# Optimization experiments

Hardware: AMD Instinct MI355X
Metric: run time of the kernel (lower is better)

Reference implementation:

```python
import jax, jax.numpy as jnp
import numpy as np

NEG_SLOPE = 0.2
EPS = 1e-16


def _add_self_loops(edge_index, edge_weight, N):
    # PyG add_self_loops with fill_value='mean': self-loop attr = mean of
    # incoming edge attrs per node (0 if node has no incoming edges).
    src, dst = edge_index[0], edge_index[1]
    ones = jnp.ones_like(edge_weight)
    cnt = jax.ops.segment_sum(ones, dst, num_segments=N)
    wsum = jax.ops.segment_sum(edge_weight, dst, num_segments=N)
    self_w = jnp.where(cnt > 0, wsum / jnp.maximum(cnt, 1.0), 0.0)
    loop = jnp.arange(N, dtype=src.dtype)
    return (jnp.concatenate([src, loop]), jnp.concatenate([dst, loop]),
            jnp.concatenate([edge_weight, self_w]))


def _gatv2_layer(x, src, dst, ew, Wl, Wr, att, We, bias, N):
    # x: [M, N, Din]; src/dst: [E']; ew: [E']; att: [H, C]
    M = x.shape[0]
    H, C = att.shape
    xl = (x @ Wl).reshape(M, N, H, C)   # source transform (lin_l)
    xr = (x @ Wr).reshape(M, N, H, C)   # target transform (lin_r)
    xj = xl[:, src]                      # [M, E', H, C] gather source feats
    xi = xr[:, dst]                      # [M, E', H, C] gather target feats
    ee = (ew[:, None] @ We).reshape(-1, H, C)  # [E', H, C] edge embedding
    s = jax.nn.leaky_relu(xi + xj + ee[None], NEG_SLOPE)
    logits = jnp.einsum('mehc,hc->meh', s, att)  # [M, E', H]
    # segment softmax over edges grouped by destination node
    smax = jax.vmap(lambda u: jax.ops.segment_max(u, dst, num_segments=N))(logits)
    a = jnp.exp(logits - smax[:, dst])
    denom = jax.vmap(lambda u: jax.ops.segment_sum(u, dst, num_segments=N))(a)
    alpha = a / (denom[:, dst] + EPS)
    msg = alpha[..., None] * xj          # [M, E', H, C]
    out = jax.vmap(lambda u: jax.ops.segment_sum(u, dst, num_segments=N))(msg)
    return out.reshape(M, N, H * C) + bias


def setup_inputs() -> dict:
    key = jax.random.key(0)
    ks = jax.random.split(key, 14)
    B, T, N, Din = 2, 8, 5000, 64
    E, H, OUT = 80000, 2, 128
    C = OUT // H  # 64
    g = jax.nn.initializers.glorot_uniform()
    inp = {
        'x': jax.random.normal(ks[0], (B, T, N, Din), jnp.float32),
        'edge_index': jax.random.randint(ks[1], (2, E), 0, N, jnp.int32),
        'edge_weight': jax.random.uniform(ks[2], (E,), jnp.float32),
        # conv1 params
        'Wl1': g(ks[3], (Din, H * C), jnp.float32),
        'Wr1': g(ks[4], (Din, H * C), jnp.float32),
        'att1': g(ks[5], (H, C), jnp.float32),
        'We1': g(ks[6], (1, H * C), jnp.float32),
        'b1': jnp.zeros((H * C,), jnp.float32),
        # conv2 params
        'Wl2': g(ks[7], (OUT, H * C), jnp.float32),
        'Wr2': g(ks[8], (OUT, H * C), jnp.float32),
        'att2': g(ks[9], (H, C), jnp.float32),
        'We2': g(ks[10], (1, H * C), jnp.float32),
        'b2': jnp.zeros((H * C,), jnp.float32),
    }
    return inp


def reference(x, edge_index, edge_weight, Wl1, Wr1, att1, We1, b1,
              Wl2, Wr2, att2, We2, b2):
    B, T, N, Din = x.shape
    M = B * T
    # Tiling edges by B*T with node offsets is equivalent to sharing the same
    # edge list across M independent graph copies -> vectorize over M.
    src, dst, ew = _add_self_loops(edge_index, edge_weight, N)
    h = x.reshape(M, N, Din)
    h = _gatv2_layer(h, src, dst, ew, Wl1, Wr1, att1, We1, b1, N)
    h = jax.nn.elu(h)
    h = _gatv2_layer(h, src, dst, ew, Wl2, Wr2, att2, We2, b2, N)
    h = jax.nn.elu(h)
    return h.reshape(B, T, N, -1)
```

## Files before the change

kernel.cpp:

```cpp
#include <hip/hip_runtime.h>
#include <cstdint>
#include <cstddef>

static constexpr float NEG_SLOPE_C = 0.2f;
static constexpr float EPS_C = 1e-16f;
static constexpr float LOG2E_C = 1.4426950408889634f;

#if defined(__has_builtin)
#if __has_builtin(__builtin_amdgcn_exp2f)
#define EXP2F(x) __builtin_amdgcn_exp2f(x)
#else
#define EXP2F(x) exp2f(x)
#endif
#else
#define EXP2F(x) exp2f(x)
#endif

typedef __attribute__((ext_vector_type(8))) short bf16x8;
typedef __attribute__((ext_vector_type(4))) float f32x4;
typedef __attribute__((ext_vector_type(2))) float f32x2;

__device__ __forceinline__ f32x2 pk_add(f32x2 a, f32x2 b) {
    f32x2 d;
    asm("v_pk_add_f32 %0, %1, %2" : "=v"(d) : "v"(a), "v"(b));
    return d;
}
__device__ __forceinline__ f32x2 pk_mul(f32x2 a, f32x2 b) {
    f32x2 d;
    asm("v_pk_mul_f32 %0, %1, %2" : "=v"(d) : "v"(a), "v"(b));
    return d;
}
__device__ __forceinline__ f32x2 pk_fma(f32x2 a, f32x2 b, f32x2 c) {
    f32x2 d;
    asm("v_pk_fma_f32 %0, %1, %2, %3" : "=v"(d) : "v"(a), "v"(b), "v"(c));
    return d;
}
__device__ __forceinline__ f32x2 pk_abs(f32x2 a) {
    f32x2 d;
    d.x = __builtin_fabsf(a.x);
    d.y = __builtin_fabsf(a.y);
    return d;
}

__device__ __forceinline__ short bf16_rne(float x) {
    unsigned u = __float_as_uint(x);
    u = (u + 0x7FFF + ((u >> 16) & 1)) >> 16;
    return (short)u;
}
__device__ __forceinline__ float bf16f(short s) {
    return __uint_as_float(((unsigned)(unsigned short)s) << 16);
}

template<int CTRL>
__device__ __forceinline__ float dpp_add_f(float v) {
    int x = __builtin_amdgcn_update_dpp(0, __float_as_int(v), CTRL, 0xf, 0xf, true);
    return v + __int_as_float(x);
}

__device__ __forceinline__ float reduce16(float q) {
    q = dpp_add_f<0xB1>(q);
    q = dpp_add_f<0x4E>(q);
    q = dpp_add_f<0x141>(q);
    q = dpp_add_f<0x140>(q);
    return q;
}


__global__ void degree_kernel(const int* __restrict__ ei, const float* __restrict__ ew,
                              int E, int* __restrict__ cnt, float* __restrict__ wsum) {
    int e = blockIdx.x * blockDim.x + threadIdx.x;
    if (e >= E) return;
    int dst = ei[E + e];
    atomicAdd(&cnt[dst], 1);
    atomicAdd(&wsum[dst], ew[e]);
}

__global__ void scan_kernel(const int* __restrict__ cnt, const float* __restrict__ wsum,
                            int N, int E, int* __restrict__ offs, float* __restrict__ self_w) {
    __shared__ int bufA[1024];
    __shared__ int bufB[1024];
    int t = threadIdx.x;
    int chunk = (N + 1023) / 1024;
    int lo = t * chunk;
    int hi = lo + chunk; if (hi > N) hi = N; if (lo > N) lo = N;
    int s = 0;
    for (int n = lo; n < hi; ++n) s += cnt[n];
    bufA[t] = s;
    __syncthreads();
    int* srcb = bufA; int* dstb = bufB;
    for (int d = 1; d < 1024; d <<= 1) {
        int v = srcb[t];
        if (t >= d) v += srcb[t - d];
        dstb[t] = v;
        __syncthreads();
        int* tmp = srcb; srcb = dstb; dstb = tmp;
    }
    int run = (t == 0) ? 0 : srcb[t - 1];
    for (int n = lo; n < hi; ++n) { offs[n] = run; run += cnt[n]; }
    if (t == 0) offs[N] = E;
    for (int n = t; n < N; n += 1024) {
        int c = cnt[n];
        self_w[n] = (c > 0) ? (wsum[n] / (float)c) : 0.0f;
    }
}

__global__ void scatter_kernel(const int* __restrict__ ei, const float* __restrict__ ew, int E,
                               const int* __restrict__ offs, int* __restrict__ cursor,
                               int2* __restrict__ pairs) {
    int e = blockIdx.x * blockDim.x + threadIdx.x;
    if (e >= E) return;
    int dst = ei[E + e];
    int pos = offs[dst] + atomicAdd(&cursor[dst], 1);
    pairs[pos] = make_int2(ei[e] * 512, __float_as_int(ew[e]));
}


template<int K>
__global__ void wprep_kernel(const float* __restrict__ Wl, const float* __restrict__ Wr,
                             uint4* __restrict__ Wf) {
    const int gid = blockIdx.x * 256 + threadIdx.x;
    const int lane = gid & 63;
    const int t = (gid >> 6) & 15;
    const int s = gid >> 10;
    const int mr = lane & 15, q = lane >> 4;
    const int col = t * 16 + mr;
    const float* src = (col < 128) ? (Wl + col) : (Wr + col - 128);
    union { short sh[8]; uint4 u; } hv, lv;
    #pragma unroll
    for (int j = 0; j < 8; ++j) {
        const float v = src[(size_t)(s * 32 + q * 8 + j) * 128];
        const short h = bf16_rne(v);
        hv.sh[j] = h;
        lv.sh[j] = bf16_rne(v - bf16f(h));
    }
    const size_t base = (size_t)s * 2048 + (size_t)(t * 2) * 64 + lane;
    Wf[base] = hv.u;
    Wf[base + 64] = lv.u;
}


template<int K>
__global__ __launch_bounds__(256) void gemm_mfma_kernel(
    const float* __restrict__ X, const uint4* __restrict__ Wf,
    float* __restrict__ outL, float* __restrict__ outR) {
    __shared__ uint4 xbuf[8 * 64];
    const int tid = threadIdx.x;
    const int w = tid >> 6;
    const int lane = tid & 63;
    const int q = lane >> 4;
    const int mr = lane & 15;
    const int blockRow = blockIdx.x * 64;

    const int srow = lane;
    const float* sxp = X + (size_t)(blockRow + srow) * K + w * 8;
    const int sdst = ((srow >> 4) * 2) * 64 + w * 16 + (srow & 15);

    f32x4 acc[4][4];
    #pragma unroll
    for (int tt = 0; tt < 4; ++tt)
        #pragma unroll
        for (int r = 0; r < 4; ++r)
            acc[tt][r] = (f32x4){0.f, 0.f, 0.f, 0.f};

    for (int s = 0; s < K / 32; ++s) {
        const float4 a0 = *(const float4*)(sxp + s * 32);
        const float4 a1 = *(const float4*)(sxp + s * 32 + 4);
        union { short sh[8]; uint4 u; } hv, lv;
        {
            const float av[8] = {a0.x, a0.y, a0.z, a0.w, a1.x, a1.y, a1.z, a1.w};
            #pragma unroll
            for (int jj = 0; jj < 8; ++jj) {
                const short h = bf16_rne(av[jj]);
                hv.sh[jj] = h;
                lv.sh[jj] = bf16_rne(av[jj] - bf16f(h));
            }
        }
        __syncthreads();
        xbuf[sdst] = hv.u;
        xbuf[sdst + 64] = lv.u;
        __syncthreads();

        bf16x8 xh[4], xl[4];
        #pragma unroll
        for (int r = 0; r < 4; ++r) {
            xh[r] = *(const bf16x8*)&xbuf[(r * 2) * 64 + lane];
            xl[r] = *(const bf16x8*)&xbuf[(r * 2 + 1) * 64 + lane];
        }
        const uint4* wp = Wf + (size_t)s * 2048 + (size_t)(4 * w) * 128 + lane;
        #pragma unroll
        for (int tt = 0; tt < 4; ++tt) {
            const bf16x8 wh = *(const bf16x8*)&wp[tt * 128];
            const bf16x8 wl = *(const bf16x8*)&wp[tt * 128 + 64];
            #pragma unroll
            for (int r = 0; r < 4; ++r) {
                acc[tt][r] = __builtin_amdgcn_mfma_f32_16x16x32_bf16(wh, xh[r], acc[tt][r], 0, 0, 0);
                acc[tt][r] = __builtin_amdgcn_mfma_f32_16x16x32_bf16(wl, xh[r], acc[tt][r], 0, 0, 0);
                acc[tt][r] = __builtin_amdgcn_mfma_f32_16x16x32_bf16(wh, xl[r], acc[tt][r], 0, 0, 0);
            }
        }
    }

    float* const obase = (w < 2) ? outL : outR;
    const int cbase = (w & 1) * 64 + q * 4;
    #pragma unroll
    for (int tt = 0; tt < 4; ++tt) {
        #pragma unroll
        for (int r = 0; r < 4; ++r) {
            const size_t o = (size_t)(blockRow + r * 16 + mr) * 128 + cbase + tt * 16;
            *(float4*)(obase + o) =
                make_float4(acc[tt][r][0], acc[tt][r][1], acc[tt][r][2], acc[tt][r][3]);
        }
    }
}


__global__ __launch_bounds__(256) void edge_kernel(
    const float* __restrict__ xl, const float* __restrict__ xr,
    const int* __restrict__ offs, const int2* __restrict__ pairs,
    const float* __restrict__ self_w,
    const float* __restrict__ att, const float* __restrict__ We,
    const float* __restrict__ bias, float* __restrict__ out,
    int N, int M) {
    const int wave = __builtin_amdgcn_readfirstlane(threadIdx.x >> 6);
    const int b = blockIdx.x;
    const int hb = (b >= 10000) ? (b - 10000) : b;
    const int m = ((b >= 10000) ? 8 : 0) + (hb & 7);
    const int n = (hb >> 3) * 4 + wave;
    if (n >= N) return;
    const int lane = threadIdx.x & 63;
    const int j = lane & 31;
    const bool hi = lane >= 32;
    const int h4 = (lane >> 5) << 2;
    const int j16 = j << 4;

    const char* xlp = (const char*)(xl + (size_t)m * N * 128);
    const char* xrp = (const char*)(xr + (size_t)m * N * 128);

    const int beg = offs[n], end = offs[n + 1];
    const int last = end - 1;
    const bool any = end > beg;

    int2 myp;
    if (any) myp = pairs[min(beg + lane, last)];

    f32x2 a06_01, a06_23, a04_01, a04_23, we01, we23, xi01, xi23;
    {
        const float4 at4 = ((const float4*)att)[j];
        const float4 we4 = ((const float4*)We)[j];
        const float4 xi4 = *(const float4*)(xrp + (size_t)n * 512 + j16);
        const float c06 = 0.6f * LOG2E_C, c04 = 0.4f * LOG2E_C;
        a06_01 = (f32x2){at4.x * c06, at4.y * c06};
        a06_23 = (f32x2){at4.z * c06, at4.w * c06};
        a04_01 = (f32x2){at4.x * c04, at4.y * c04};
        a04_23 = (f32x2){at4.z * c04, at4.w * c04};
        we01 = (f32x2){we4.x, we4.y};
        we23 = (f32x2){we4.z, we4.w};
        xi01 = (f32x2){xi4.x, xi4.y};
        xi23 = (f32x2){xi4.z, xi4.w};
    }

    float base, lsum;
    f32x2 acc01, acc23;
    {
        const float sw = self_w[n];
        const f32x2 sw2 = (f32x2){sw, sw};
        const float4 xj4 = *(const float4*)(xlp + (size_t)n * 512 + j16);
        const f32x2 s01 = pk_fma(sw2, we01, pk_add(xi01, (f32x2){xj4.x, xj4.y}));
        const f32x2 s23 = pk_fma(sw2, we23, pk_add(xi23, (f32x2){xj4.z, xj4.w}));
        f32x2 q01 = pk_mul(a06_01, s01);
        q01 = pk_fma(a04_01, pk_abs(s01), q01);
        f32x2 q23 = pk_mul(a06_23, s23);
        q23 = pk_fma(a04_23, pk_abs(s23), q23);
        const f32x2 qp = pk_add(q01, q23);
        base = reduce16(qp.x + qp.y);
        lsum = 0.5f;
        acc01 = (f32x2){xj4.x * 0.5f, xj4.y * 0.5f};
        acc23 = (f32x2){xj4.z * 0.5f, xj4.w * 0.5f};
    }

    auto BODY = [&](f32x2 w2, float4 xj4, bool mask) {
        const f32x2 xj01 = (f32x2){xj4.x, xj4.y};
        const f32x2 xj23 = (f32x2){xj4.z, xj4.w};
        const f32x2 s01 = pk_fma(w2, we01, pk_add(xi01, xj01));
        const f32x2 s23 = pk_fma(w2, we23, pk_add(xi23, xj23));
        f32x2 q01 = pk_mul(a06_01, s01);
        q01 = pk_fma(a04_01, pk_abs(s01), q01);
        f32x2 q23 = pk_mul(a06_23, s23);
        q23 = pk_fma(a04_23, pk_abs(s23), q23);
        const f32x2 qp = pk_add(q01, q23);
        const float q = reduce16(qp.x + qp.y);
        float t = EXP2F(q - base);
        if (mask) t = hi ? 0.f : t;
        lsum += t;
        const f32x2 t2 = (f32x2){t, t};
        acc01 = pk_fma(t2, xj01, acc01);
        acc23 = pk_fma(t2, xj23, acc23);
    };

    if (any) {
        for (int cbeg = beg; cbeg < end; cbeg += 64) {
            const int cdeg = min(end - cbeg, 64);
            const int niter = (cdeg + 1) >> 1;
            const bool odd = (cdeg & 1) != 0;

            auto PULL = [&](int s, int& ro, f32x2& w2) {
                const int idx = (s << 3) + h4;
                ro = __builtin_amdgcn_ds_bpermute(idx, myp.x);
                const int wb = __builtin_amdgcn_ds_bpermute(idx, myp.y);
                w2.x = __int_as_float(wb);
                w2.y = w2.x;
            };
            auto GATH = [&](int ro) -> float4 {
                return *(const float4*)(xlp + (unsigned)(ro + j16));
            };

            int roA, roB, roC, roD;
            f32x2 wA, wB, wC, wD;
            PULL(0, roA, wA);
            PULL(1, roB, wB);
            PULL(2, roC, wC);
            PULL(3, roD, wD);
            float4 xA = GATH(roA);
            float4 xB = GATH(roB);
            float4 xC, xD;

            int k = 0;
            while (k + 4 < niter) {
                xC = GATH(roC);
                xD = GATH(roD);
                __builtin_amdgcn_sched_barrier(0);
                BODY(wA, xA, false);
                PULL(k + 4, roA, wA);
                BODY(wB, xB, false);
                PULL(k + 5, roB, wB);
                xA = GATH(roA);
                xB = GATH(roB);
                __builtin_amdgcn_sched_barrier(0);
                BODY(wC, xC, false);
                PULL(k + 6, roC, wC);
                BODY(wD, xD, false);
                PULL(k + 7, roD, wD);
                k += 4;
            }
            const int rem = niter - k;
            if (rem >= 3) xC = GATH(roC);
            if (rem == 4) xD = GATH(roD);
            BODY(wA, xA, odd && (rem == 1));
            if (rem >= 2) BODY(wB, xB, odd && (rem == 2));
            if (rem >= 3) BODY(wC, xC, odd && (rem == 3));
            if (rem == 4) BODY(wD, xD, odd);

            if (cbeg + 64 < end)
                myp = pairs[min(cbeg + 64 + lane, last)];
        }
    }

    lsum += __shfl_xor(lsum, 32, 64);
    acc01.x += __shfl_xor(acc01.x, 32, 64);
    acc01.y += __shfl_xor(acc01.y, 32, 64);
    acc23.x += __shfl_xor(acc23.x, 32, 64);
    acc23.y += __shfl_xor(acc23.y, 32, 64);

    const float inv = 1.f / (lsum + EPS_C);
    const float4 b4 = ((const float4*)bias)[j];
    float o0 = fmaf(acc01.x, inv, b4.x);
    float o1 = fmaf(acc01.y, inv, b4.y);
    float o2 = fmaf(acc23.x, inv, b4.z);
    float o3 = fmaf(acc23.y, inv, b4.w);
    o0 = o0 > 0.f ? o0 : (__expf(o0) - 1.f);
    o1 = o1 > 0.f ? o1 : (__expf(o1) - 1.f);
    o2 = o2 > 0.f ? o2 : (__expf(o2) - 1.f);
    o3 = o3 > 0.f ? o3 : (__expf(o3) - 1.f);
    if (!hi) {
        ((float4*)(out + (size_t)m * N * 128))[n * 32 + j] =
            make_float4(o0, o1, o2, o3);
    }
}


extern "C" void kernel_launch(void* const* d_in, const int* in_sizes, int n_in,
                              void* d_out, int out_size, void* d_ws, size_t ws_size,
                              hipStream_t stream) {
    const float* x    = (const float*)d_in[0];
    const int*   ei   = (const int*)d_in[1];
    const float* ew   = (const float*)d_in[2];
    const float* Wl1  = (const float*)d_in[3];
    const float* Wr1  = (const float*)d_in[4];
    const float* att1 = (const float*)d_in[5];
    const float* We1  = (const float*)d_in[6];
    const float* b1   = (const float*)d_in[7];
    const float* Wl2  = (const float*)d_in[8];
    const float* Wr2  = (const float*)d_in[9];
    const float* att2 = (const float*)d_in[10];
    const float* We2  = (const float*)d_in[11];
    const float* b2   = (const float*)d_in[12];

    const int E = in_sizes[1] / 2;
    const int N = 5000;
    const int R = out_size / 128;
    const int M = R / N;

    char* ws = (char*)d_ws;
    size_t off = 0;
    auto alloc = [&](size_t bytes) {
        char* p = ws + off;
        off = (off + bytes + 255) & ~(size_t)255;
        return p;
    };
    int*   cnt    = (int*)  alloc((size_t)N * 4);
    float* wsum   = (float*)alloc((size_t)N * 4);
    int*   cursor = (int*)  alloc((size_t)N * 4);
    float* selfw  = (float*)alloc((size_t)N * 4);
    int*   offs   = (int*)  alloc((size_t)(N + 1) * 4);
    int2*  pairs  = (int2*) alloc((size_t)(E + 1) * 8);
    uint4* wf1    = (uint4*)alloc((size_t)2 * 2048 * 16);
    uint4* wf2    = (uint4*)alloc((size_t)4 * 2048 * 16);
    float* bufA   = (float*)alloc((size_t)R * 128 * 4);
    float* bufB   = (float*)alloc((size_t)R * 128 * 4);
    float* bufC   = (float*)alloc((size_t)R * 128 * 4);

    const size_t zspan = (size_t)((char*)cursor - (char*)cnt) + (size_t)N * 4;
    hipMemsetAsync(cnt, 0, zspan, stream);

    int eb = (E + 255) / 256;
    degree_kernel<<<eb, 256, 0, stream>>>(ei, ew, E, cnt, wsum);
    scan_kernel<<<1, 1024, 0, stream>>>(cnt, wsum, N, E, offs, selfw);
    scatter_kernel<<<eb, 256, 0, stream>>>(ei, ew, E, offs, cursor, pairs);
    wprep_kernel<64><<<8, 256, 0, stream>>>(Wl1, Wr1, wf1);
    wprep_kernel<128><<<16, 256, 0, stream>>>(Wl2, Wr2, wf2);

    const int gb = R / 64;
    const int tb = 2 * ((N + 3) / 4) * 8;

    gemm_mfma_kernel<64><<<gb, 256, 0, stream>>>(x, wf1, bufA, bufB);
    edge_kernel<<<tb, 256, 0, stream>>>(bufA, bufB, offs, pairs, selfw,
                                        att1, We1, b1, bufC, N, M);
    gemm_mfma_kernel<128><<<gb, 256, 0, stream>>>(bufC, wf2, bufA, bufB);
    edge_kernel<<<tb, 256, 0, stream>>>(bufA, bufB, offs, pairs, selfw,
                                        att2, We2, b2, (float*)d_out, N, M);
}
```

Before: 283.7 us.

## Process two graph copies per wave in edge kernel and merge weight prep launches

Each wave in the edge kernel now handles two batch slices (m and m+8) for the same destination node. The CSR offsets, edge pairs, permutes, attention and edge-weight setup are therefore shared across both slices, and the number of independent gathers in flight doubles. The grid is halved to match. The two weight-prep launches are merged into one to save a launch. The trade-off is more registers per thread, which may lower occupancy.

Measured after the change: 284.8 us. Within noise of the previous version (+0.4%).

```diff
diff --git a/kernel.cpp b/kernel.cpp
--- a/kernel.cpp
+++ b/kernel.cpp
@@ -115,10 +115,9 @@
 }
 
 
-template<int K>
-__global__ void wprep_kernel(const float* __restrict__ Wl, const float* __restrict__ Wr,
-                             uint4* __restrict__ Wf) {
-    const int gid = blockIdx.x * 256 + threadIdx.x;
+__device__ __forceinline__ void wprep_body(const float* __restrict__ Wl,
+                                           const float* __restrict__ Wr,
+                                           uint4* __restrict__ Wf, int gid) {
     const int lane = gid & 63;
     const int t = (gid >> 6) & 15;
     const int s = gid >> 10;
@@ -136,6 +135,15 @@
     const size_t base = (size_t)s * 2048 + (size_t)(t * 2) * 64 + lane;
     Wf[base] = hv.u;
     Wf[base + 64] = lv.u;
+}
+
+__global__ void wprep_all_kernel(const float* __restrict__ Wl1, const float* __restrict__ Wr1,
+                                 uint4* __restrict__ wf1,
+                                 const float* __restrict__ Wl2, const float* __restrict__ Wr2,
+                                 uint4* __restrict__ wf2) {
+    const int blk = blockIdx.x;
+    if (blk < 8) wprep_body(Wl1, Wr1, wf1, blk * 256 + threadIdx.x);
+    else         wprep_body(Wl2, Wr2, wf2, (blk - 8) * 256 + threadIdx.x);
 }
 
 
@@ -223,9 +231,9 @@
     int N, int M) {
     const int wave = __builtin_amdgcn_readfirstlane(threadIdx.x >> 6);
     const int b = blockIdx.x;
-    const int hb = (b >= 10000) ? (b - 10000) : b;
-    const int m = ((b >= 10000) ? 8 : 0) + (hb & 7);
-    const int n = (hb >> 3) * 4 + wave;
+    const int m0 = b & 7;
+    const int m1 = m0 + 8;
+    const int n = (b >> 3) * 4 + wave;
     if (n >= N) return;
     const int lane = threadIdx.x & 63;
     const int j = lane & 31;
@@ -233,8 +241,10 @@
     const int h4 = (lane >> 5) << 2;
     const int j16 = j << 4;
 
-    const char* xlp = (const char*)(xl + (size_t)m * N * 128);
-    const char* xrp = (const char*)(xr + (size_t)m * N * 128);
+    const char* xlp0 = (const char*)(xl + (size_t)m0 * N * 128);
+    const char* xlp1 = (const char*)(xl + (size_t)m1 * N * 128);
+    const char* xrp0 = (const char*)(xr + (size_t)m0 * N * 128);
+    const char* xrp1 = (const char*)(xr + (size_t)m1 * N * 128);
 
     const int beg = offs[n], end = offs[n + 1];
     const int last = end - 1;
@@ -243,11 +253,11 @@
     int2 myp;
     if (any) myp = pairs[min(beg + lane, last)];
 
-    f32x2 a06_01, a06_23, a04_01, a04_23, we01, we23, xi01, xi23;
+    f32x2 a06_01, a06_23, a04_01, a04_23, we01, we23;
+    f32x2 xi01_0, xi23_0, xi01_1, xi23_1;
     {
         const float4 at4 = ((const float4*)att)[j];
         const float4 we4 = ((const float4*)We)[j];
-        const float4 xi4 = *(const float4*)(xrp + (size_t)n * 512 + j16);
         const float c06 = 0.6f * LOG2E_C, c04 = 0.4f * LOG2E_C;
         a06_01 = (f32x2){at4.x * c06, at4.y * c06};
         a06_23 = (f32x2){at4.z * c06, at4.w * c06};
@@ -255,46 +265,57 @@
         a04_23 = (f32x2){at4.z * c04, at4.w * c04};
         we01 = (f32x2){we4.x, we4.y};
         we23 = (f32x2){we4.z, we4.w};
-        xi01 = (f32x2){xi4.x, xi4.y};
-        xi23 = (f32x2){xi4.z, xi4.w};
-    }
-
-    float base, lsum;
-    f32x2 acc01, acc23;
-    {
-        const float sw = self_w[n];
-        const f32x2 sw2 = (f32x2){sw, sw};
-        const float4 xj4 = *(const float4*)(xlp + (size_t)n * 512 + j16);
-        const f32x2 s01 = pk_fma(sw2, we01, pk_add(xi01, (f32x2){xj4.x, xj4.y}));
-        const f32x2 s23 = pk_fma(sw2, we23, pk_add(xi23, (f32x2){xj4.z, xj4.w}));
+        const float4 xiA = *(const float4*)(xrp0 + (size_t)n * 512 + j16);
+        const float4 xiB = *(const float4*)(xrp1 + (size_t)n * 512 + j16);
+        xi01_0 = (f32x2){xiA.x, xiA.y};
+        xi23_0 = (f32x2){xiA.z, xiA.w};
+        xi01_1 = (f32x2){xiB.x, xiB.y};
+        xi23_1 = (f32x2){xiB.z, xiB.w};
+    }
+
+    auto SCORE = [&](f32x2 w2, f32x2 xi01, f32x2 xi23, float4 xj4) -> f32x2 {
+        const f32x2 s01 = pk_fma(w2, we01, pk_add(xi01, (f32x2){xj4.x, xj4.y}));
+        const f32x2 s23 = pk_fma(w2, we23, pk_add(xi23, (f32x2){xj4.z, xj4.w}));
         f32x2 q01 = pk_mul(a06_01, s01);
         q01 = pk_fma(a04_01, pk_abs(s01), q01);
         f32x2 q23 = pk_mul(a06_23, s23);
         q23 = pk_fma(a04_23, pk_abs(s23), q23);
-        const f32x2 qp = pk_add(q01, q23);
-        base = reduce16(qp.x + qp.y);
-        lsum = 0.5f;
-        acc01 = (f32x2){xj4.x * 0.5f, xj4.y * 0.5f};
-        acc23 = (f32x2){xj4.z * 0.5f, xj4.w * 0.5f};
-    }
-
-    auto BODY = [&](f32x2 w2, float4 xj4, bool mask) {
-        const f32x2 xj01 = (f32x2){xj4.x, xj4.y};
-        const f32x2 xj23 = (f32x2){xj4.z, xj4.w};
-        const f32x2 s01 = pk_fma(w2, we01, pk_add(xi01, xj01));
-        const f32x2 s23 = pk_fma(w2, we23, pk_add(xi23, xj23));
-        f32x2 q01 = pk_mul(a06_01, s01);
-        q01 = pk_fma(a04_01, pk_abs(s01), q01);
-        f32x2 q23 = pk_mul(a06_23, s23);
-        q23 = pk_fma(a04_23, pk_abs(s23), q23);
-        const f32x2 qp = pk_add(q01, q23);
-        const float q = reduce16(qp.x + qp.y);
-        float t = EXP2F(q - base);
-        if (mask) t = hi ? 0.f : t;
-        lsum += t;
-        const f32x2 t2 = (f32x2){t, t};
-        acc01 = pk_fma(t2, xj01, acc01);
-        acc23 = pk_fma(t2, xj23, acc23);
+        return pk_add(q01, q23);
+    };
+
+    float base0, base1, lsum0, lsum1;
+    f32x2 acc01_0, acc23_0, acc01_1, acc23_1;
+    {
+        const float sw = self_w[n];
+        const f32x2 sw2 = (f32x2){sw, sw};
+        const float4 xj0 = *(const float4*)(xlp0 + (size_t)n * 512 + j16);
+        const float4 xj1 = *(const float4*)(xlp1 + (size_t)n * 512 + j16);
+        const f32x2 qp0 = SCORE(sw2, xi01_0, xi23_0, xj0);
+        const f32x2 qp1 = SCORE(sw2, xi01_1, xi23_1, xj1);
+        base0 = reduce16(qp0.x + qp0.y);
+        base1 = reduce16(qp1.x + qp1.y);
+        lsum0 = 0.5f;
+        lsum1 = 0.5f;
+        acc01_0 = (f32x2){xj0.x * 0.5f, xj0.y * 0.5f};
+        acc23_0 = (f32x2){xj0.z * 0.5f, xj0.w * 0.5f};
+        acc01_1 = (f32x2){xj1.x * 0.5f, xj1.y * 0.5f};
+        acc23_1 = (f32x2){xj1.z * 0.5f, xj1.w * 0.5f};
+    }
+
+    auto BODY = [&](f32x2 w2, float4 xj0, float4 xj1, bool mask) {
+        const f32x2 qp0 = SCORE(w2, xi01_0, xi23_0, xj0);
+        const f32x2 qp1 = SCORE(w2, xi01_1, xi23_1, xj1);
+        const float q0 = reduce16(qp0.x + qp0.y);
+        const float q1 = reduce16(qp1.x + qp1.y);
+        float t0 = EXP2F(q0 - base0);
+        float t1 = EXP2F(q1 - base1);
+        if (mask) { t0 = hi ? 0.f : t0; t1 = hi ? 0.f : t1; }
+        lsum0 += t0;
+        lsum1 += t1;
+        acc01_0 = pk_fma((f32x2){t0, t0}, (f32x2){xj0.x, xj0.y}, acc01_0);
+        acc23_0 = pk_fma((f32x2){t0, t0}, (f32x2){xj0.z, xj0.w}, acc23_0);
+        acc01_1 = pk_fma((f32x2){t1, t1}, (f32x2){xj1.x, xj1.y}, acc01_1);
+        acc23_1 = pk_fma((f32x2){t1, t1}, (f32x2){xj1.z, xj1.w}, acc23_1);
     };
 
     if (any) {
@@ -310,8 +331,11 @@
                 w2.x = __int_as_float(wb);
                 w2.y = w2.x;
             };
-            auto GATH = [&](int ro) -> float4 {
-                return *(const float4*)(xlp + (unsigned)(ro + j16));
+            auto G0 = [&](int ro) -> float4 {
+                return *(const float4*)(xlp0 + (unsigned)(ro + j16));
+            };
+            auto G1 = [&](int ro) -> float4 {
+                return *(const float4*)(xlp1 + (unsigned)(ro + j16));
             };
 
             int roA, roB, roC, roD;
@@ -320,60 +344,77 @@
             PULL(1, roB, wB);
             PULL(2, roC, wC);
             PULL(3, roD, wD);
-            float4 xA = GATH(roA);
-            float4 xB = GATH(roB);
-            float4 xC, xD;
+            float4 xA0 = G0(roA), xA1 = G1(roA);
+            float4 xB0 = G0(roB), xB1 = G1(roB);
+            float4 xC0, xC1, xD0, xD1;
 
             int k = 0;
             while (k + 4 < niter) {
-                xC = GATH(roC);
-                xD = GATH(roD);
+                xC0 = G0(roC); xC1 = G1(roC);
+                xD0 = G0(roD); xD1 = G1(roD);
                 __builtin_amdgcn_sched_barrier(0);
-                BODY(wA, xA, false);
+                BODY(wA, xA0, xA1, false);
                 PULL(k + 4, roA, wA);
-                BODY(wB, xB, false);
+                BODY(wB, xB0, xB1, false);
                 PULL(k + 5, roB, wB);
-                xA = GATH(roA);
-                xB = GATH(roB);
+                xA0 = G0(roA); xA1 = G1(roA);
+                xB0 = G0(roB); xB1 = G1(roB);
                 __builtin_amdgcn_sched_barrier(0);
-                BODY(wC, xC, false);
+                BODY(wC, xC0, xC1, false);
                 PULL(k + 6, roC, wC);
-                BODY(wD, xD, false);
+                BODY(wD, xD0, xD1, false);
                 PULL(k + 7, roD, wD);
                 k += 4;
             }
             const int rem = niter - k;
-            if (rem >= 3) xC = GATH(roC);
-            if (rem == 4) xD = GATH(roD);
-            BODY(wA, xA, odd && (rem == 1));
-            if (rem >= 2) BODY(wB, xB, odd && (rem == 2));
-            if (rem >= 3) BODY(wC, xC, odd && (rem == 3));
-            if (rem == 4) BODY(wD, xD, odd);
+            if (rem >= 3) { xC0 = G0(roC); xC1 = G1(roC); }
+            if (rem == 4) { xD0 = G0(roD); xD1 = G1(roD); }
+            BODY(wA, xA0, xA1, odd && (rem == 1));
+            if (rem >= 2) BODY(wB, xB0, xB1, odd && (rem == 2));
+            if (rem >= 3) BODY(wC, xC0, xC1, odd && (rem == 3));
+            if (rem == 4) BODY(wD, xD0, xD1, odd);
 
             if (cbeg + 64 < end)
                 myp = pairs[min(cbeg + 64 + lane, last)];
         }
     }
 
-    lsum += __shfl_xor(lsum, 32, 64);
-    acc01.x += __shfl_xor(acc01.x, 32, 64);
-    acc01.y += __shfl_xor(acc01.y, 32, 64);
-    acc23.x += __shfl_xor(acc23.x, 32, 64);
-    acc23.y += __shfl_xor(acc23.y, 32, 64);
-
-    const float inv = 1.f / (lsum + EPS_C);
+    lsum0 += __shfl_xor(lsum0, 32, 64);
+    lsum1 += __shfl_xor(lsum1, 32, 64);
+    acc01_0.x += __shfl_xor(acc01_0.x, 32, 64);
+    acc01_0.y += __shfl_xor(acc01_0.y, 32, 64);
+    acc23_0.x += __shfl_xor(acc23_0.x, 32, 64);
+    acc23_0.y += __shfl_xor(acc23_0.y, 32, 64);
+    acc01_1.x += __shfl_xor(acc01_1.x, 32, 64);
+    acc01_1.y += __shfl_xor(acc01_1.y, 32, 64);
+    acc23_1.x += __shfl_xor(acc23_1.x, 32, 64);
+    acc23_1.y += __shfl_xor(acc23_1.y, 32, 64);
+
     const float4 b4 = ((const float4*)bias)[j];
-    float o0 = fmaf(acc01.x, inv, b4.x);
-    float o1 = fmaf(acc01.y, inv, b4.y);
-    float o2 = fmaf(acc23.x, inv, b4.z);
-    float o3 = fmaf(acc23.y, inv, b4.w);
-    o0 = o0 > 0.f ? o0 : (__expf(o0) - 1.f);
-    o1 = o1 > 0.f ? o1 : (__expf(o1) - 1.f);
-    o2 = o2 > 0.f ? o2 : (__expf(o2) - 1.f);
-    o3 = o3 > 0.f ? o3 : (__expf(o3) - 1.f);
     if (!hi) {
-        ((float4*)(out + (size_t)m * N * 128))[n * 32 + j] =
+        const float inv0 = 1.f / (lsum0 + EPS_C);
+        float o0 = fmaf(acc01_0.x, inv0, b4.x);
+        float o1 = fmaf(acc01_0.y, inv0, b4.y);
+        float o2 = fmaf(acc23_0.x, inv0, b4.z);
+        float o3 = fmaf(acc23_0.y, inv0, b4.w);
+        o0 = o0 > 0.f ? o0 : (__expf(o0) - 1.f);
+        o1 = o1 > 0.f ? o1 : (__expf(o1) - 1.f);
+        o2 = o2 > 0.f ? o2 : (__expf(o2) - 1.f);
+        o3 = o3 > 0.f ? o3 : (__expf(o3) - 1.f);
+        ((float4*)(out + (size_t)m0 * N * 128))[n * 32 + j] =
             make_float4(o0, o1, o2, o3);
+
+        const float inv1 = 1.f / (lsum1 + EPS_C);
+        float p0 = fmaf(acc01_1.x, inv1, b4.x);
+        float p1 = fmaf(acc01_1.y, inv1, b4.y);
+        float p2 = fmaf(acc23_1.x, inv1, b4.z);
+        float p3 = fmaf(acc23_1.y, inv1, b4.w);
+        p0 = p0 > 0.f ? p0 : (__expf(p0) - 1.f);
+        p1 = p1 > 0.f ? p1 : (__expf(p1) - 1.f);
+        p2 = p2 > 0.f ? p2 : (__expf(p2) - 1.f);
+        p3 = p3 > 0.f ? p3 : (__expf(p3) - 1.f);
+        ((float4*)(out + (size_t)m1 * N * 128))[n * 32 + j] =
+            make_float4(p0, p1, p2, p3);
     }
 }
 
@@ -426,11 +467,10 @@
     degree_kernel<<<eb, 256, 0, stream>>>(ei, ew, E, cnt, wsum);
     scan_kernel<<<1, 1024, 0, stream>>>(cnt, wsum, N, E, offs, selfw);
     scatter_kernel<<<eb, 256, 0, stream>>>(ei, ew, E, offs, cursor, pairs);
-    wprep_kernel<64><<<8, 256, 0, stream>>>(Wl1, Wr1, wf1);
-    wprep_kernel<128><<<16, 256, 0, stream>>>(Wl2, Wr2, wf2);
+    wprep_all_kernel<<<24, 256, 0, stream>>>(Wl1, Wr1, wf1, Wl2, Wr2, wf2);
 
     const int gb = R / 64;
-    const int tb = 2 * ((N + 3) / 4) * 8;
+    const int tb = ((N + 3) / 4) * 8;
 
     gemm_mfma_kernel<64><<<gb, 256, 0, stream>>>(x, wf1, bufA, bufB);
     edge_kernel<<<tb, 256, 0, stream>>>(bufA, bufB, offs, pairs, selfw,
```
